# Performance work log

Hardware: AMD Instinct MI355X
Metric: run time of the kernel (lower is better)

The kernel has to match this reference:

```python
import jax, jax.numpy as jnp
import numpy as np
from jax import lax

EMBED_DIM = 128
HIDDEN = 50
KS = 7
BN_EPS = 1e-5


def setup_inputs() -> dict:
    key = jax.random.key(0)
    ks = jax.random.split(key, 8)
    B, L, D, H = 4, 512, EMBED_DIM, HIDDEN
    x1 = jax.random.normal(ks[0], (B, L, D), jnp.float32)
    x2 = jax.random.normal(ks[1], (B, L, D), jnp.float32)
    # conv1 (1x1) weight stored as [H, 2D] (spatial dims of size 1 dropped)
    conv1_w = jax.random.normal(ks[2], (H, 2 * D), jnp.float32) * (1.0 / np.sqrt(2 * D))
    conv1_b = jnp.zeros((H,), jnp.float32)
    bn1_g = jnp.ones((H,), jnp.float32)
    bn1_b = jnp.zeros((H,), jnp.float32)
    w2 = jax.random.normal(ks[3], (1, H, KS, KS), jnp.float32) * (1.0 / np.sqrt(H * KS * KS))
    conv2_w = 0.5 * (w2 + jnp.swapaxes(w2, 2, 3))  # clip(): symmetrize kernel
    conv2_b = jnp.zeros((1,), jnp.float32)
    bn2_g = jnp.ones((1,), jnp.float32)
    bn2_b = jnp.zeros((1,), jnp.float32)
    return {"x1": x1, "x2": x2, "conv1_w": conv1_w, "conv1_b": conv1_b,
            "bn1_g": bn1_g, "bn1_b": bn1_b, "conv2_w": conv2_w, "conv2_b": conv2_b,
            "bn2_g": bn2_g, "bn2_b": bn2_b}


def _batch_norm(x, g, b):
    # train-mode BN: batch statistics over (N, H, W), biased variance (PyTorch)
    m = jnp.mean(x, axis=(0, 2, 3), keepdims=True)
    v = jnp.var(x, axis=(0, 2, 3), keepdims=True)
    xn = (x - m) * lax.rsqrt(v + BN_EPS)
    return xn * g[None, :, None, None] + b[None, :, None, None]


def reference(x1, x2, conv1_w, conv1_b, bn1_g, bn1_b, conv2_w, conv2_b, bn2_g, bn2_b):
    # x1, x2: [B, L, D] -> channel-first [B, D, L]
    x1c = jnp.swapaxes(x1, 1, 2)
    x2c = jnp.swapaxes(x2, 1, 2)
    D = x1c.shape[1]
    w_dif, w_mul = conv1_w[:, :D], conv1_w[:, D:]
    # 1x1 conv over concat([|x1_i - x2_j|, x1_i * x2_j]) fused as two contractions
    dif = jnp.abs(x1c[:, :, :, None] - x2c[:, :, None, :])        # [B, D, L1, L2]
    h = jnp.einsum('bdij,hd->bhij', dif, w_dif)
    h = h + jnp.einsum('bdi,bdj,hd->bhij', x1c, x2c, w_mul)       # mul term, no [B,D,L,L] materialized by hand
    h = h + conv1_b[None, :, None, None]
    h = jax.nn.relu(h)                 # activation1 BEFORE batch_norm1 (as in source)
    h = _batch_norm(h, bn1_g, bn1_b)
    # conv2: symmetric 7x7, padding ks//2 == SAME for odd ks
    y = lax.conv_general_dilated(h, conv2_w, window_strides=(1, 1), padding='SAME',
                                 dimension_numbers=('NCHW', 'OIHW', 'NCHW'))
    y = y + conv2_b[None, :, None, None]
    y = _batch_norm(y, bn2_g, bn2_b)
    y = jax.nn.sigmoid(y)
    return y[:, 0, :, :]               # squeeze channel -> [B, L1, L2]
```

## Files before the change

kernel.cpp:

```cpp
#include <hip/hip_runtime.h>

#define LL 512
#define DD 128
#define HH 50
#define JW 520

typedef short v8s __attribute__((ext_vector_type(8)));
typedef float f32x4 __attribute__((ext_vector_type(4)));
typedef float f32x2 __attribute__((ext_vector_type(2)));
typedef unsigned int u32x4 __attribute__((ext_vector_type(4)));

__device__ __forceinline__ unsigned cvtpk(float a, float b) {
  unsigned r;
  asm("v_cvt_pk_bf16_f32 %0, %1, %2" : "=v"(r) : "v"(a), "v"(b));
  return r;
}
__device__ __forceinline__ unsigned cvtpkabs(float a, float b) {
  unsigned r;
  asm("v_cvt_pk_bf16_f32 %0, abs(%1), abs(%2)" : "=v"(r) : "v"(a), "v"(b));
  return r;
}
__device__ __forceinline__ unsigned short f2bf(float f) {
  unsigned u = __builtin_bit_cast(unsigned, f);
  u = (u + 0x7fffu + ((u >> 16) & 1u)) >> 16;
  return (unsigned short)u;
}
__device__ __forceinline__ void gload16(const void* g, void* l) {
  __builtin_amdgcn_global_load_lds(
      (const __attribute__((address_space(1))) unsigned int*)g,
      (__attribute__((address_space(3))) unsigned int*)l, 16, 0, 0);
}

__global__ void pass0(const float* __restrict__ c1w, unsigned short* __restrict__ wbuf)
{
  const int idx = blockIdx.x * 256 + threadIdx.x;
  const int r = idx >> 8;
  wbuf[idx] = f2bf((r < HH) ? c1w[idx] : 0.f);
}

__global__ __launch_bounds__(256, 2) void pass1(
    const float* __restrict__ x1, const float* __restrict__ x2,
    const unsigned short* __restrict__ wbuf, const float* __restrict__ c1b,
    unsigned short* __restrict__ hbuf, float* __restrict__ partials)
{
  __shared__ unsigned short wlin[64 * 256];
  __shared__ float x1s[32 * 128];

  const int tid = threadIdx.x;
  const int wv = tid >> 6, lane = tid & 63;
  const int lh = lane & 15, lg = lane >> 4;
  const int bx = blockIdx.x, by = blockIdx.y, bz = blockIdx.z;
  const int j0 = bx << 6, i0 = by << 5;

#pragma unroll
  for (int k = 0; k < 8; ++k)
    gload16(wbuf + (((k << 8) + tid) << 3), wlin + ((((k << 2) + wv) << 6) << 3));
  {
    const float* x1base = x1 + (size_t)(bz * LL + i0) * DD;
#pragma unroll
    for (int k = 0; k < 4; ++k)
      gload16(x1base + (((k << 8) + tid) << 2), x1s + ((((k << 2) + wv) << 6) << 2));
  }
  __syncthreads();

  v8s bfr[4][8];
  {
    const unsigned wbase = (unsigned)(size_t)
        ((__attribute__((address_space(3))) char*)&wlin[0]);
#pragma unroll
    for (int n = 0; n < 4; n++)
#pragma unroll
      for (int kt = 0; kt < 8; kt++) {
        unsigned off = wbase + (unsigned)((((n * 16 + lh) << 8) + kt * 32 + lg * 8) << 1);
        asm volatile("ds_read_b128 %0, %1" : "=v"(bfr[n][kt]) : "v"(off));
      }
    asm volatile("s_waitcnt lgkmcnt(0)" ::: "memory");
    __builtin_amdgcn_sched_barrier(0);
  }

  f32x2 x2p[4][4];
  {
    const int j = j0 + (wv << 4) + lh;
    const float* g = x2 + ((size_t)(bz * LL + j) * DD + (lg << 3));
#pragma unroll
    for (int kt = 0; kt < 4; kt++)
#pragma unroll
      for (int m = 0; m < 4; m++)
        x2p[kt][m] = *(const f32x2*)(g + kt * 32 + 2 * m);
  }
  f32x2 bias2[4][2];
#pragma unroll
  for (int n = 0; n < 4; n++)
#pragma unroll
    for (int h2 = 0; h2 < 2; h2++) {
      int h0 = n * 16 + (lg << 2) + 2 * h2;
      bias2[n][h2] = f32x2{(h0 < HH) ? c1b[h0] : 0.f,
                           (h0 + 1 < HH) ? c1b[h0 + 1] : 0.f};
    }

  f32x2 ssum2[4][2], ssq2[4][2];
#pragma unroll
  for (int n = 0; n < 4; n++)
#pragma unroll
    for (int h2 = 0; h2 < 2; h2++) {
      ssum2[n][h2] = f32x2{0.f, 0.f};
      ssq2[n][h2] = f32x2{0.f, 0.f};
    }

  unsigned short* hb = hbuf +
      ((size_t)(bz * LL + i0) * JW + 4 + j0 + (wv << 4) + lh) * 64 + (lg << 2);

#pragma unroll 2
  for (int di = 0; di < 32; ++di) {
    f32x4 acc[4];
#pragma unroll
    for (int n = 0; n < 4; n++) acc[n] = f32x4{0.f, 0.f, 0.f, 0.f};
#pragma unroll
    for (int kt = 0; kt < 4; ++kt) {
      const float* xr = &x1s[(di << 7) + kt * 32 + (lg << 3)];
      u32x4 ad, am;
#pragma unroll
      for (int m = 0; m < 4; m++) {
        f32x2 xp = *(const f32x2*)(xr + 2 * m);
        f32x2 d = xp - x2p[kt][m];
        f32x2 pr = xp * x2p[kt][m];
        ad[m] = cvtpkabs(d[0], d[1]);
        am[m] = cvtpk(pr[0], pr[1]);
      }
      v8s vad = __builtin_bit_cast(v8s, ad);
      v8s vam = __builtin_bit_cast(v8s, am);
#pragma unroll
      for (int n = 0; n < 4; n++)
        acc[n] = __builtin_amdgcn_mfma_f32_16x16x32_bf16(bfr[n][kt], vad, acc[n], 0, 0, 0);
#pragma unroll
      for (int n = 0; n < 4; n++)
        acc[n] = __builtin_amdgcn_mfma_f32_16x16x32_bf16(bfr[n][kt + 4], vam, acc[n], 0, 0, 0);
    }
    unsigned short* hp = hb + (size_t)di * (JW * 64);
#pragma unroll
    for (int n = 0; n < 4; ++n) {
      f32x2 v0 = f32x2{acc[n][0], acc[n][1]} + bias2[n][0];
      f32x2 v1 = f32x2{acc[n][2], acc[n][3]} + bias2[n][1];
      v0 = __builtin_elementwise_max(v0, f32x2{0.f, 0.f});
      v1 = __builtin_elementwise_max(v1, f32x2{0.f, 0.f});
      ssum2[n][0] += v0; ssum2[n][1] += v1;
      ssq2[n][0] += v0 * v0; ssq2[n][1] += v1 * v1;
      unsigned lo = cvtpk(v0[0], v0[1]), hi = cvtpk(v1[0], v1[1]);
      *(unsigned long long*)(hp + n * 16) = ((unsigned long long)hi << 32) | lo;
    }
  }

  __syncthreads();
  float* stred = x1s;
#pragma unroll
  for (int n = 0; n < 4; ++n)
#pragma unroll
    for (int q = 0; q < 4; ++q) {
      float s = ssum2[n][q >> 1][q & 1], t = ssq2[n][q >> 1][q & 1];
#pragma unroll
      for (int m = 1; m < 16; m <<= 1) { s += __shfl_xor(s, m); t += __shfl_xor(t, m); }
      if (lh == 0) {
        stred[(wv << 7) + n * 16 + (lg << 2) + q] = s;
        stred[(wv << 7) + 64 + n * 16 + (lg << 2) + q] = t;
      }
    }
  __syncthreads();
  if (tid < 128) {
    int bid = (bz * gridDim.y + by) * gridDim.x + bx;
    partials[bid * 128 + tid] = stred[tid] + stred[128 + tid] + stred[256 + tid] + stred[384 + tid];
  }

  if (bx == 0 || bx == 7) {
    const int jb = (bx == 0) ? 0 : 516;
#pragma unroll
    for (int k = 0; k < 4; ++k) {
      int unit = tid + (k << 8);
      int ii = unit >> 5;
      int rem = unit & 31;
      int jj = jb + (rem >> 3);
      int ch = (rem & 7) << 3;
      u32x4 z = {0u, 0u, 0u, 0u};
      *(u32x4*)&hbuf[((size_t)(bz * LL + i0 + ii) * JW + jj) * 64 + ch] = z;
    }
  }
}

__global__ void pass2a(const float* __restrict__ partials, float* __restrict__ red1)
{
  __shared__ float acc2[2][128];
  const int tid = threadIdx.x, b = blockIdx.x;
  const int slot = tid & 127, half = tid >> 7;
  float s = 0.f;
#pragma unroll
  for (int k = 0; k < 4; k++)
    s += partials[(b * 8 + half * 4 + k) * 128 + slot];
  acc2[half][slot] = s;
  __syncthreads();
  if (tid < 128) red1[b * 128 + tid] = acc2[0][tid] + acc2[1][tid];
}

__global__ void pass2b(const float* __restrict__ red1,
                       const float* __restrict__ c2w, const float* __restrict__ c2b,
                       const float* __restrict__ bn1g, const float* __restrict__ bn1b,
                       unsigned short* __restrict__ wA, float* __restrict__ tmap)
{
  __shared__ float acc2[2][128];
  __shared__ float sq[128];
  __shared__ float aa[64], cc[64];
  __shared__ float wlds[2450];
  __shared__ float tpart[49][5];
  const int tid = threadIdx.x;
  const int slot = tid & 127, half = tid >> 7;
  float s = 0.f;
#pragma unroll
  for (int k = 0; k < 32; k++) s += red1[(half * 32 + k) * 128 + slot];
  acc2[half][slot] = s;
  __syncthreads();
  if (tid < 128) sq[tid] = acc2[0][tid] + acc2[1][tid];
  for (int i = tid; i < 2450; i += 256) wlds[i] = c2w[i];
  __syncthreads();
  if (tid < HH) {
    float S = sq[tid], Q = sq[64 + tid];
    const float N = 4.0f * 512.f * 512.f;
    float m = S / N, v = fmaxf(Q / N - m * m, 0.f);
    float a = bn1g[tid] * rsqrtf(v + 1e-5f);
    aa[tid] = a;
    cc[tid] = bn1b[tid] - m * a;
  }
  __syncthreads();
  for (int idx = tid; idx < 16 * 448; idx += 256) {
    int ky = idx / 448, r = idx - ky * 448;
    int kx = r >> 6, ch = r & 63;
    float v = (ky < 7 && ch < HH) ? aa[ch] * wlds[ch * 49 + ky * 7 + kx] : 0.f;
    wA[idx] = f2bf(v);
  }
  if (tid < 245) {
    int c = tid / 5, g = tid - (tid / 5) * 5;
    int ci = c / 7, cj = c - (c / 7) * 7;
    int kylo = ci < 3 ? 3 - ci : 0, kyhi = ci > 3 ? 9 - ci : 6;
    int kxlo = cj < 3 ? 3 - cj : 0, kxhi = cj > 3 ? 9 - cj : 6;
    float t = 0.f;
    for (int h = g * 10; h < g * 10 + 10; h++) {
      float sm = 0.f;
      for (int ky = kylo; ky <= kyhi; ky++)
        for (int kx = kxlo; kx <= kxhi; kx++) sm += wlds[h * 49 + ky * 7 + kx];
      t += cc[h] * sm;
    }
    tpart[c][g] = t;
  }
  __syncthreads();
  if (tid < 49)
    tmap[tid] = c2b[0] + tpart[tid][0] + tpart[tid][1] + tpart[tid][2]
              + tpart[tid][3] + tpart[tid][4];
}

__global__ __launch_bounds__(256, 3) void pass3(
    const unsigned short* __restrict__ hbuf, const unsigned short* __restrict__ wA,
    const float* __restrict__ tmap, float* __restrict__ ybuf, float* __restrict__ part2)
{
  __shared__ unsigned short T[2][72 * 64];
  __shared__ float tm[49];
  __shared__ float rs[4], rq[4];

  const int tid = threadIdx.x;
  const int wv = tid >> 6, lane = tid & 63;
  const int lh = lane & 15, lg = lane >> 4;
  const int bx = blockIdx.x, by = blockIdx.y, bz = blockIdx.z;
  const int j0 = bx << 6, i0 = by << 4;

  v8s afr[14];
#pragma unroll
  for (int kt = 0; kt < 14; kt++)
    afr[kt] = *(const v8s*)&wA[lh * 448 + kt * 32 + (lg << 3)];

  if (tid < 49) tm[tid] = tmap[tid];

  const int jc = (wv << 4) + lh;
  float ya[4] = {0.f, 0.f, 0.f, 0.f};

  auto stage = [&](int buf, int row) {
    const unsigned short* rowp = hbuf + ((size_t)(bz * LL + row) * JW + j0) * 64;
#pragma unroll
    for (int cc2 = 0; cc2 < 2; ++cc2) {
      const int c = wv + (cc2 << 2);
      const int u = (c << 6) + lane;
      const int tj = u >> 3, oct = u & 7;
      gload16(rowp + tj * 64 + ((oct ^ (tj & 7)) << 3), &T[buf][c << 9]);
    }
    if (wv == 0) {
      const int u = 512 + lane;
      const int tj = u >> 3, oct = u & 7;
      gload16(rowp + tj * 64 + ((oct ^ (tj & 7)) << 3), &T[buf][8 << 9]);
    }
  };

  { const int r0 = i0 - 3; if (r0 >= 0) stage(0, r0); }
  __syncthreads();

  for (int rb = 0; rb < 24; rb += 8) {
#pragma unroll
    for (int u8 = 0; u8 < 8; ++u8) {
      const int rr = rb + u8;
      const int r = i0 - 3 + rr;
      const int cur = rr & 1;
      if (rr + 1 < 22) {
        const int rn = r + 1;
        if (rn >= 0 && rn < LL) stage(cur ^ 1, rn);
      }
      if (rr < 22 && r >= 0 && r < LL) {
        f32x4 a0 = {0.f, 0.f, 0.f, 0.f}, a1 = {0.f, 0.f, 0.f, 0.f};
#pragma unroll
        for (int kt = 0; kt < 14; ++kt) {
          const int kx = kt >> 1;
          const int t = jc + 1 + kx;
          const int sl = ((kt & 1) << 2) + lg;
          v8s b = *(const v8s*)&T[cur][(t << 6) + ((sl ^ (t & 7)) << 3)];
          if (kt & 1) a1 = __builtin_amdgcn_mfma_f32_16x16x32_bf16(afr[kt], b, a1, 0, 0, 0);
          else        a0 = __builtin_amdgcn_mfma_f32_16x16x32_bf16(afr[kt], b, a0, 0, 0, 0);
        }
        float zq[4];
#pragma unroll
        for (int q = 0; q < 4; ++q) zq[q] = a0[q] + a1[q];
#pragma unroll
        for (int ky = 0; ky < 7; ++ky) {
          float zz = __shfl(zq[ky & 3], ((ky >> 2) << 4) + lh, 64);
          const int idx = rr - ky;
          const bool ok = ((unsigned)idx < 16u) && ((idx >> 2) == lg);
          ya[(u8 - ky) & 3] += ok ? zz : 0.f;
        }
      }
      __syncthreads();
    }
  }

  float sa = 0.f, qa = 0.f;
  const int jj = j0 + jc;
  const int cj = jj < 3 ? jj : (jj > 508 ? jj - 505 : 3);
#pragma unroll
  for (int s = 0; s < 4; ++s) {
    const int i = i0 + (lg << 2) + s;
    const int ci = i < 3 ? i : (i > 508 ? i - 505 : 3);
    float v = ya[s] + tm[ci * 7 + cj];
    ybuf[(size_t)(bz * LL + i) * LL + jj] = v;
    sa += v; qa += v * v;
  }
#pragma unroll
  for (int m = 1; m < 64; m <<= 1) { sa += __shfl_xor(sa, m); qa += __shfl_xor(qa, m); }
  if (lane == 0) { rs[wv] = sa; rq[wv] = qa; }
  __syncthreads();
  if (tid == 0) {
    const int bid = (bz * gridDim.y + by) * gridDim.x + bx;
    part2[bid] = rs[0] + rs[1] + rs[2] + rs[3];
    part2[1024 + bid] = rq[0] + rq[1] + rq[2] + rq[3];
  }
}

__global__ void pass3b(const float* __restrict__ part2, float* __restrict__ stats2)
{
  __shared__ float rs[4], rq[4];
  const int tid = threadIdx.x;
  float s = 0.f, q = 0.f;
  for (int i = tid; i < 1024; i += 256) { s += part2[i]; q += part2[1024 + i]; }
#pragma unroll
  for (int m = 1; m < 64; m <<= 1) { s += __shfl_xor(s, m); q += __shfl_xor(q, m); }
  const int wave = tid >> 6, lane = tid & 63;
  if (lane == 0) { rs[wave] = s; rq[wave] = q; }
  __syncthreads();
  if (tid == 0) {
    float S = rs[0] + rs[1] + rs[2] + rs[3];
    float Q = rq[0] + rq[1] + rq[2] + rq[3];
    const float N = 4.0f * 512.f * 512.f;
    float m2 = S / N, v2 = fmaxf(Q / N - m2 * m2, 0.f);
    stats2[0] = m2;
    stats2[1] = rsqrtf(v2 + 1e-5f);
  }
}

__global__ void pass4(const float* __restrict__ y, const float* __restrict__ stats2,
                      const float* __restrict__ bn2g, const float* __restrict__ bn2b,
                      float* __restrict__ out)
{
  const int idx = blockIdx.x * 256 + threadIdx.x;
  const float m2 = stats2[0], inv = stats2[1];
  const float g = bn2g[0], b = bn2b[0];
  f32x4 v = ((const f32x4*)y)[idx];
  f32x4 r;
#pragma unroll
  for (int e = 0; e < 4; e++) {
    float xn = (v[e] - m2) * inv * g + b;
    r[e] = 1.f / (1.f + __expf(-xn));
  }
  ((f32x4*)out)[idx] = r;
}

extern "C" void kernel_launch(void* const* d_in, const int* in_sizes, int n_in,
                              void* d_out, int out_size, void* d_ws, size_t ws_size,
                              hipStream_t stream) {
  (void)in_sizes; (void)n_in; (void)out_size; (void)ws_size;
  const float* x1   = (const float*)d_in[0];
  const float* x2   = (const float*)d_in[1];
  const float* c1w  = (const float*)d_in[2];
  const float* c1b  = (const float*)d_in[3];
  const float* bn1g = (const float*)d_in[4];
  const float* bn1b = (const float*)d_in[5];
  const float* c2w  = (const float*)d_in[6];
  const float* c2b  = (const float*)d_in[7];
  const float* bn2g = (const float*)d_in[8];
  const float* bn2b = (const float*)d_in[9];

  char* ws = (char*)d_ws;
  float* partials       = (float*)(ws + 0);
  float* red1           = (float*)(ws + 524288);
  float* part2          = (float*)(ws + 557056);
  unsigned short* wA    = (unsigned short*)(ws + 565248);
  float* tmap           = (float*)(ws + 579584);
  float* stats2         = (float*)(ws + 579840);
  unsigned short* wbuf  = (unsigned short*)(ws + 581632);
  float* ybuf           = (float*)(ws + 1048576);
  unsigned short* hbuf  = (unsigned short*)(ws + 5242880);

  pass0<<<64, 256, 0, stream>>>(c1w, wbuf);
  pass1<<<dim3(8, 16, 4), 256, 0, stream>>>(x1, x2, wbuf, c1b, hbuf, partials);
  pass2a<<<64, 256, 0, stream>>>(partials, red1);
  pass2b<<<1, 256, 0, stream>>>(red1, c2w, c2b, bn1g, bn1b, wA, tmap);
  pass3<<<dim3(8, 32, 4), 256, 0, stream>>>(hbuf, wA, tmap, ybuf, part2);
  pass3b<<<1, 256, 0, stream>>>(part2, stats2);
  pass4<<<1024, 256, 0, stream>>>(ybuf, stats2, bn2g, bn2b, (float*)d_out);
}
```

Before: 126.0 us.

## Triple-buffer conv2 row staging, use vmcnt waits, and swizzle pass1 weight LDS

Pass3 moves from a double-buffered to a triple-buffered LDS ring for the row tiles. Loads are issued two rows ahead, and each step uses a partial vmcnt wait plus a raw s_barrier instead of a full __syncthreads, so global loads overlap with MFMA work. Out-of-range rows are clamped and still loaded, so control flow is branch-free, and invalid rows are masked in the accumulation. Pass0 and pass1 XOR-swizzle the weight layout to cut LDS bank conflicts on the ds_read_b128 fragment loads. Occupancy is raised to 4 blocks, at the cost of more LDS and extra redundant loads at the edges.

```diff
diff --git a/kernel.cpp b/kernel.cpp
--- a/kernel.cpp
+++ b/kernel.cpp
@@ -34,8 +34,8 @@
 __global__ void pass0(const float* __restrict__ c1w, unsigned short* __restrict__ wbuf)
 {
   const int idx = blockIdx.x * 256 + threadIdx.x;
-  const int r = idx >> 8;
-  wbuf[idx] = f2bf((r < HH) ? c1w[idx] : 0.f);
+  const int r = idx >> 8, c = idx & 255;
+  wbuf[(r << 8) | (c ^ ((r & 7) << 3))] = f2bf((r < HH) ? c1w[idx] : 0.f);
 }
 
 __global__ __launch_bounds__(256, 2) void pass1(
@@ -71,7 +71,9 @@
     for (int n = 0; n < 4; n++)
 #pragma unroll
       for (int kt = 0; kt < 8; kt++) {
-        unsigned off = wbase + (unsigned)((((n * 16 + lh) << 8) + kt * 32 + lg * 8) << 1);
+        const int row = n * 16 + lh;
+        const int col = (kt * 32 + lg * 8) ^ ((row & 7) << 3);
+        unsigned off = wbase + (unsigned)(((row << 8) + col) << 1);
         asm volatile("ds_read_b128 %0, %1" : "=v"(bfr[n][kt]) : "v"(off));
       }
     asm volatile("s_waitcnt lgkmcnt(0)" ::: "memory");
@@ -254,11 +256,11 @@
               + tpart[tid][3] + tpart[tid][4];
 }
 
-__global__ __launch_bounds__(256, 3) void pass3(
+__global__ __launch_bounds__(256, 4) void pass3(
     const unsigned short* __restrict__ hbuf, const unsigned short* __restrict__ wA,
     const float* __restrict__ tmap, float* __restrict__ ybuf, float* __restrict__ part2)
 {
-  __shared__ unsigned short T[2][72 * 64];
+  __shared__ unsigned short T[3][72 * 64];
   __shared__ float tm[49];
   __shared__ float rs[4], rq[4];
 
@@ -278,61 +280,65 @@
   const int jc = (wv << 4) + lh;
   float ya[4] = {0.f, 0.f, 0.f, 0.f};
 
+  auto clampr = [](int r) { return r < 0 ? 0 : (r > LL - 1 ? LL - 1 : r); };
+
   auto stage = [&](int buf, int row) {
     const unsigned short* rowp = hbuf + ((size_t)(bz * LL + row) * JW + j0) * 64;
 #pragma unroll
-    for (int cc2 = 0; cc2 < 2; ++cc2) {
-      const int c = wv + (cc2 << 2);
+    for (int c2 = 0; c2 < 2; ++c2) {
+      const int c = wv + (c2 << 2);
       const int u = (c << 6) + lane;
       const int tj = u >> 3, oct = u & 7;
       gload16(rowp + tj * 64 + ((oct ^ (tj & 7)) << 3), &T[buf][c << 9]);
     }
-    if (wv == 0) {
+    {
       const int u = 512 + lane;
       const int tj = u >> 3, oct = u & 7;
       gload16(rowp + tj * 64 + ((oct ^ (tj & 7)) << 3), &T[buf][8 << 9]);
     }
   };
 
-  { const int r0 = i0 - 3; if (r0 >= 0) stage(0, r0); }
-  __syncthreads();
-
-  for (int rb = 0; rb < 24; rb += 8) {
-#pragma unroll
-    for (int u8 = 0; u8 < 8; ++u8) {
-      const int rr = rb + u8;
+  stage(0, clampr(i0 - 3));
+  stage(1, clampr(i0 - 2));
+  asm volatile("s_waitcnt vmcnt(3) lgkmcnt(0)" ::: "memory");
+  __builtin_amdgcn_sched_barrier(0);
+  asm volatile("s_barrier" ::: "memory");
+
+  for (int rb = 0; rb < 24; rb += 12) {
+#pragma unroll
+    for (int u = 0; u < 12; ++u) {
+      const int rr = rb + u;
+      const int cur = u % 3;
+      stage((u + 2) % 3, clampr(i0 - 1 + rr));
       const int r = i0 - 3 + rr;
-      const int cur = rr & 1;
-      if (rr + 1 < 22) {
-        const int rn = r + 1;
-        if (rn >= 0 && rn < LL) stage(cur ^ 1, rn);
+      const bool rv = (rr < 22) && (r >= 0) && (r < LL);
+      f32x4 a0 = {0.f, 0.f, 0.f, 0.f}, a1 = {0.f, 0.f, 0.f, 0.f};
+#pragma unroll
+      for (int kt = 0; kt < 14; ++kt) {
+        const int kx = kt >> 1;
+        const int t = jc + 1 + kx;
+        const int sl = ((kt & 1) << 2) + lg;
+        v8s b = *(const v8s*)&T[cur][(t << 6) + ((sl ^ (t & 7)) << 3)];
+        if (kt & 1) a1 = __builtin_amdgcn_mfma_f32_16x16x32_bf16(afr[kt], b, a1, 0, 0, 0);
+        else        a0 = __builtin_amdgcn_mfma_f32_16x16x32_bf16(afr[kt], b, a0, 0, 0, 0);
       }
-      if (rr < 22 && r >= 0 && r < LL) {
-        f32x4 a0 = {0.f, 0.f, 0.f, 0.f}, a1 = {0.f, 0.f, 0.f, 0.f};
-#pragma unroll
-        for (int kt = 0; kt < 14; ++kt) {
-          const int kx = kt >> 1;
-          const int t = jc + 1 + kx;
-          const int sl = ((kt & 1) << 2) + lg;
-          v8s b = *(const v8s*)&T[cur][(t << 6) + ((sl ^ (t & 7)) << 3)];
-          if (kt & 1) a1 = __builtin_amdgcn_mfma_f32_16x16x32_bf16(afr[kt], b, a1, 0, 0, 0);
-          else        a0 = __builtin_amdgcn_mfma_f32_16x16x32_bf16(afr[kt], b, a0, 0, 0, 0);
-        }
-        float zq[4];
-#pragma unroll
-        for (int q = 0; q < 4; ++q) zq[q] = a0[q] + a1[q];
-#pragma unroll
-        for (int ky = 0; ky < 7; ++ky) {
-          float zz = __shfl(zq[ky & 3], ((ky >> 2) << 4) + lh, 64);
-          const int idx = rr - ky;
-          const bool ok = ((unsigned)idx < 16u) && ((idx >> 2) == lg);
-          ya[(u8 - ky) & 3] += ok ? zz : 0.f;
-        }
+      float zq[4];
+#pragma unroll
+      for (int q = 0; q < 4; ++q) zq[q] = a0[q] + a1[q];
+#pragma unroll
+      for (int ky = 0; ky < 7; ++ky) {
+        float zz = __shfl(zq[ky & 3], ((ky >> 2) << 4) + lh, 64);
+        const int idx = rr - ky;
+        const bool ok = rv && ((unsigned)idx < 16u) && ((idx >> 2) == lg);
+        ya[(u - ky) & 3] += ok ? zz : 0.f;
       }
-      __syncthreads();
-    }
-  }
-
+      asm volatile("s_waitcnt vmcnt(3)" ::: "memory");
+      __builtin_amdgcn_sched_barrier(0);
+      asm volatile("s_barrier" ::: "memory");
+    }
+  }
+
+  __syncthreads();
   float sa = 0.f, qa = 0.f;
   const int jj = j0 + jc;
   const int cj = jj < 3 ? jj : (jj > 508 ? jj - 505 : 3);
```

New measurement: 128.0 us. About the same (+1.6%).

## Fold small reduction and weight-prep kernels into neighbors to cut launches

Applied to the files above, without the earlier changes.

Removes three tiny kernels: the conv1 weight bf16 conversion moves into pass1 (each block converts and XOR-swizzles the weights into LDS), the two-stage BN1 reduction becomes one single-block kernel, and the BN2 stats reduction is recomputed redundantly by every block of pass4. The aim is to cut launch and inter-kernel gaps in a pipeline of short passes. In exchange, every pass1 block redoes the weight conversion, the single-block pass2 reads all 512 partials serially, and every pass4 block re-reduces 1024 partials. pass3 launch bounds also rise to 4 blocks per CU.

```diff
diff --git a/kernel.cpp b/kernel.cpp
--- a/kernel.cpp
+++ b/kernel.cpp
@@ -31,16 +31,9 @@
       (__attribute__((address_space(3))) unsigned int*)l, 16, 0, 0);
 }
 
-__global__ void pass0(const float* __restrict__ c1w, unsigned short* __restrict__ wbuf)
-{
-  const int idx = blockIdx.x * 256 + threadIdx.x;
-  const int r = idx >> 8;
-  wbuf[idx] = f2bf((r < HH) ? c1w[idx] : 0.f);
-}
-
 __global__ __launch_bounds__(256, 2) void pass1(
     const float* __restrict__ x1, const float* __restrict__ x2,
-    const unsigned short* __restrict__ wbuf, const float* __restrict__ c1b,
+    const float* __restrict__ c1w, const float* __restrict__ c1b,
     unsigned short* __restrict__ hbuf, float* __restrict__ partials)
 {
   __shared__ unsigned short wlin[64 * 256];
@@ -52,14 +45,23 @@
   const int bx = blockIdx.x, by = blockIdx.y, bz = blockIdx.z;
   const int j0 = bx << 6, i0 = by << 5;
 
-#pragma unroll
-  for (int k = 0; k < 8; ++k)
-    gload16(wbuf + (((k << 8) + tid) << 3), wlin + ((((k << 2) + wv) << 6) << 3));
   {
     const float* x1base = x1 + (size_t)(bz * LL + i0) * DD;
 #pragma unroll
     for (int k = 0; k < 4; ++k)
       gload16(x1base + (((k << 8) + tid) << 2), x1s + ((((k << 2) + wv) << 6) << 2));
+  }
+  {
+#pragma unroll
+    for (int it = 0; it < 16; ++it) {
+      int flat = (it * 256 + tid) << 2;
+      int row = flat >> 8, col = flat & 255;
+      f32x4 v = (row < HH) ? *(const f32x4*)(c1w + flat) : f32x4{0.f, 0.f, 0.f, 0.f};
+      unsigned lo = cvtpk(v[0], v[1]), hi = cvtpk(v[2], v[3]);
+      int scol = col ^ ((row & 7) << 3);
+      *(unsigned long long*)&wlin[(row << 8) + scol] =
+          ((unsigned long long)hi << 32) | lo;
+    }
   }
   __syncthreads();
 
@@ -71,7 +73,9 @@
     for (int n = 0; n < 4; n++)
 #pragma unroll
       for (int kt = 0; kt < 8; kt++) {
-        unsigned off = wbase + (unsigned)((((n * 16 + lh) << 8) + kt * 32 + lg * 8) << 1);
+        const int row = n * 16 + lh;
+        const int col = (kt * 32 + lg * 8) ^ ((row & 7) << 3);
+        unsigned off = wbase + (unsigned)(((row << 8) + col) << 1);
         asm volatile("ds_read_b128 %0, %1" : "=v"(bfr[n][kt]) : "v"(off));
       }
     asm volatile("s_waitcnt lgkmcnt(0)" ::: "memory");
@@ -185,24 +189,10 @@
   }
 }
 
-__global__ void pass2a(const float* __restrict__ partials, float* __restrict__ red1)
-{
-  __shared__ float acc2[2][128];
-  const int tid = threadIdx.x, b = blockIdx.x;
-  const int slot = tid & 127, half = tid >> 7;
-  float s = 0.f;
-#pragma unroll
-  for (int k = 0; k < 4; k++)
-    s += partials[(b * 8 + half * 4 + k) * 128 + slot];
-  acc2[half][slot] = s;
-  __syncthreads();
-  if (tid < 128) red1[b * 128 + tid] = acc2[0][tid] + acc2[1][tid];
-}
-
-__global__ void pass2b(const float* __restrict__ red1,
-                       const float* __restrict__ c2w, const float* __restrict__ c2b,
-                       const float* __restrict__ bn1g, const float* __restrict__ bn1b,
-                       unsigned short* __restrict__ wA, float* __restrict__ tmap)
+__global__ void pass2(const float* __restrict__ partials,
+                      const float* __restrict__ c2w, const float* __restrict__ c2b,
+                      const float* __restrict__ bn1g, const float* __restrict__ bn1b,
+                      unsigned short* __restrict__ wA, float* __restrict__ tmap)
 {
   __shared__ float acc2[2][128];
   __shared__ float sq[128];
@@ -212,8 +202,9 @@
   const int tid = threadIdx.x;
   const int slot = tid & 127, half = tid >> 7;
   float s = 0.f;
-#pragma unroll
-  for (int k = 0; k < 32; k++) s += red1[(half * 32 + k) * 128 + slot];
+#pragma unroll 4
+  for (int k = 0; k < 256; k++)
+    s += partials[((half * 256 + k) << 7) + slot];
   acc2[half][slot] = s;
   __syncthreads();
   if (tid < 128) sq[tid] = acc2[0][tid] + acc2[1][tid];
@@ -254,7 +245,7 @@
               + tpart[tid][3] + tpart[tid][4];
 }
 
-__global__ __launch_bounds__(256, 3) void pass3(
+__global__ __launch_bounds__(256, 4) void pass3(
     const unsigned short* __restrict__ hbuf, const unsigned short* __restrict__ wA,
     const float* __restrict__ tmap, float* __restrict__ ybuf, float* __restrict__ part2)
 {
@@ -281,8 +272,8 @@
   auto stage = [&](int buf, int row) {
     const unsigned short* rowp = hbuf + ((size_t)(bz * LL + row) * JW + j0) * 64;
 #pragma unroll
-    for (int cc2 = 0; cc2 < 2; ++cc2) {
-      const int c = wv + (cc2 << 2);
+    for (int c2 = 0; c2 < 2; ++c2) {
+      const int c = wv + (c2 << 2);
       const int u = (c << 6) + lane;
       const int tj = u >> 3, oct = u & 7;
       gload16(rowp + tj * 64 + ((oct ^ (tj & 7)) << 3), &T[buf][c << 9]);
@@ -355,34 +346,31 @@
   }
 }
 
-__global__ void pass3b(const float* __restrict__ part2, float* __restrict__ stats2)
+__global__ void pass4(const float* __restrict__ y, const float* __restrict__ part2,
+                      const float* __restrict__ bn2g, const float* __restrict__ bn2b,
+                      float* __restrict__ out)
 {
   __shared__ float rs[4], rq[4];
   const int tid = threadIdx.x;
+  const int wave = tid >> 6, lane = tid & 63;
   float s = 0.f, q = 0.f;
-  for (int i = tid; i < 1024; i += 256) { s += part2[i]; q += part2[1024 + i]; }
+#pragma unroll
+  for (int k = 0; k < 4; ++k) {
+    int i = tid + (k << 8);
+    s += part2[i]; q += part2[1024 + i];
+  }
 #pragma unroll
   for (int m = 1; m < 64; m <<= 1) { s += __shfl_xor(s, m); q += __shfl_xor(q, m); }
-  const int wave = tid >> 6, lane = tid & 63;
   if (lane == 0) { rs[wave] = s; rq[wave] = q; }
   __syncthreads();
-  if (tid == 0) {
-    float S = rs[0] + rs[1] + rs[2] + rs[3];
-    float Q = rq[0] + rq[1] + rq[2] + rq[3];
-    const float N = 4.0f * 512.f * 512.f;
-    float m2 = S / N, v2 = fmaxf(Q / N - m2 * m2, 0.f);
-    stats2[0] = m2;
-    stats2[1] = rsqrtf(v2 + 1e-5f);
-  }
-}
-
-__global__ void pass4(const float* __restrict__ y, const float* __restrict__ stats2,
-                      const float* __restrict__ bn2g, const float* __restrict__ bn2b,
-                      float* __restrict__ out)
-{
-  const int idx = blockIdx.x * 256 + threadIdx.x;
-  const float m2 = stats2[0], inv = stats2[1];
+  const float S = rs[0] + rs[1] + rs[2] + rs[3];
+  const float Q = rq[0] + rq[1] + rq[2] + rq[3];
+  const float N = 4.0f * 512.f * 512.f;
+  const float m2 = S / N;
+  const float inv = rsqrtf(fmaxf(Q / N - m2 * m2, 0.f) + 1e-5f);
   const float g = bn2g[0], b = bn2b[0];
+
+  const int idx = blockIdx.x * 256 + tid;
   f32x4 v = ((const f32x4*)y)[idx];
   f32x4 r;
 #pragma unroll
@@ -410,20 +398,14 @@
 
   char* ws = (char*)d_ws;
   float* partials       = (float*)(ws + 0);
-  float* red1           = (float*)(ws + 524288);
   float* part2          = (float*)(ws + 557056);
   unsigned short* wA    = (unsigned short*)(ws + 565248);
   float* tmap           = (float*)(ws + 579584);
-  float* stats2         = (float*)(ws + 579840);
-  unsigned short* wbuf  = (unsigned short*)(ws + 581632);
   float* ybuf           = (float*)(ws + 1048576);
   unsigned short* hbuf  = (unsigned short*)(ws + 5242880);
 
-  pass0<<<64, 256, 0, stream>>>(c1w, wbuf);
-  pass1<<<dim3(8, 16, 4), 256, 0, stream>>>(x1, x2, wbuf, c1b, hbuf, partials);
-  pass2a<<<64, 256, 0, stream>>>(partials, red1);
-  pass2b<<<1, 256, 0, stream>>>(red1, c2w, c2b, bn1g, bn1b, wA, tmap);
+  pass1<<<dim3(8, 16, 4), 256, 0, stream>>>(x1, x2, c1w, c1b, hbuf, partials);
+  pass2<<<1, 256, 0, stream>>>(partials, c2w, c2b, bn1g, bn1b, wA, tmap);
   pass3<<<dim3(8, 32, 4), 256, 0, stream>>>(hbuf, wA, tmap, ybuf, part2);
-  pass3b<<<1, 256, 0, stream>>>(part2, stats2);
-  pass4<<<1024, 256, 0, stream>>>(ybuf, stats2, bn2g, bn2b, (float*)d_out);
-}
+  pass4<<<1024, 256, 0, stream>>>(ybuf, part2, bn2g, bn2b, (float*)d_out);
+}
```

Result: slower. 134.5 us (+6.7%).
